# Kernel optimization log

Measured on AMD Instinct MI355X. Metric: run time of the kernel, lower is better.

Reference implementation:

```python
import jax, jax.numpy as jnp
import numpy as np

EPS = 1e-6
B, N, M, C, H = 4, 2048, 1024, 1024, 16
HD = C // H          # 64
HID = 4 * C          # 4096
SCALE = 1.0 / np.sqrt(HD)


def _ln(x, g, b):
    m = x.mean(-1, keepdims=True)
    v = jnp.mean((x - m) ** 2, -1, keepdims=True)
    return (x - m) * jax.lax.rsqrt(v + EPS) * g + b


def _rot(x):
    # interleaved rotate: (-x2, x1) pairs (rotate_half=False path)
    x1, x2 = x[..., ::2], x[..., 1::2]
    return jnp.stack([-x2, x1], axis=-1).reshape(x.shape)


def _apply_rope(x, emb):
    # emb: [N, 2*HD] = cat(sin, cos); x: [B,H,N,HD]
    sin, cos = jnp.split(emb, 2, axis=-1)
    return x * cos + _rot(x) * sin


def _sdpa(q, k, v):
    s = jnp.einsum('bhqd,bhkd->bhqk', q, k) * SCALE
    a = jax.nn.softmax(s, axis=-1)
    return jnp.einsum('bhqk,bhkd->bhqd', a, v)


def _forward(x, ctx, rope,
             wqkv, sa_qg, sa_qb, sa_kg, sa_kb, sa_wo, sa_bo,
             ca_wq, ca_wk, ca_wv, ca_qg, ca_qb, ca_kg, ca_kb, ca_wo, ca_bo, ca_gate,
             w1g, b1g, w1x, b1x, w2, b2, ls0, ls1, ls2):
    Bx, Nx, Cx = x.shape
    Mx = ctx.shape[1]
    # ---- self attention (fused QKV, qk-norm, RoPE) ----
    qkv = (x @ wqkv).reshape(Bx, Nx, 3, H, HD).transpose(2, 0, 3, 1, 4)  # [3,B,H,N,HD]
    q, k, v = qkv[0], qkv[1], qkv[2]
    q = _ln(q, sa_qg, sa_qb)
    k = _ln(k, sa_kg, sa_kb)
    q = _apply_rope(q, rope)
    k = _apply_rope(k, rope)
    sa = _sdpa(q, k, v).transpose(0, 2, 1, 3).reshape(Bx, Nx, Cx)
    sa = sa @ sa_wo + sa_bo
    x = ls0 * sa + x
    # ---- cross attention (GQA degenerate: n_kv_heads == n_q_heads), gated ----
    q = (x @ ca_wq).reshape(Bx, Nx, H, HD).transpose(0, 2, 1, 3)
    k = (ctx @ ca_wk).reshape(Bx, Mx, H, HD).transpose(0, 2, 1, 3)
    v = (ctx @ ca_wv).reshape(Bx, Mx, H, HD).transpose(0, 2, 1, 3)
    q = _ln(q, ca_qg, ca_qb)
    k = _ln(k, ca_kg, ca_kb)
    q = _apply_rope(q, rope)  # rope on queries only; ctx has its own positions
    ca = _sdpa(q, k, v).transpose(0, 2, 1, 3).reshape(Bx, Nx, Cx)
    ca = (ca @ ca_wo + ca_bo) * jnp.tanh(ca_gate)
    x = ls1 * ca + x
    # ---- SwiGLU FFN ----
    h = jax.nn.silu(x @ w1g + b1g) * (x @ w1x + b1x)
    f = h @ w2 + b2
    x = ls2 * f + x
    return x


def setup_inputs() -> dict:
    key = jax.random.key(0)
    ks = iter(jax.random.split(key, 32))
    rn = lambda shape, s=0.02: (jax.random.normal(next(ks), shape, jnp.float32) * s)
    inp = {
        'x': jax.random.normal(next(ks), (B, N, C), jnp.float32),
        'ctx': jax.random.normal(next(ks), (B, M, C), jnp.float32),
    }
    # rotary table: cat(sin, cos), interleaved-repeated freqs -> [N, 2*HD]
    pos = jnp.arange(N, dtype=jnp.float32)
    inv = 1.0 / (10000.0 ** (jnp.arange(0, HD, 2, dtype=jnp.float32) / HD))
    ang = pos[:, None] * inv[None, :]                      # [N, HD/2]
    sin = jnp.repeat(jnp.sin(ang), 2, axis=-1)
    cos = jnp.repeat(jnp.cos(ang), 2, axis=-1)
    inp['rope'] = jnp.concatenate([sin, cos], axis=-1)
    inp.update(
        wqkv=rn((C, 3 * C)),
        sa_qg=jnp.ones((HD,)), sa_qb=jnp.zeros((HD,)),
        sa_kg=jnp.ones((HD,)), sa_kb=jnp.zeros((HD,)),
        sa_wo=rn((C, C)), sa_bo=jnp.zeros((C,)),
        ca_wq=rn((C, C)), ca_wk=rn((C, C)), ca_wv=rn((C, C)),
        ca_qg=jnp.ones((HD,)), ca_qb=jnp.zeros((HD,)),
        ca_kg=jnp.ones((HD,)), ca_kb=jnp.zeros((HD,)),
        ca_wo=rn((C, C)), ca_bo=jnp.zeros((C,)),
        ca_gate=jnp.full((C,), 0.5, jnp.float32),
        w1g=rn((C, HID)), b1g=jnp.zeros((HID,)),
        w1x=rn((C, HID)), b1x=jnp.zeros((HID,)),
        w2=rn((HID, C)), b2=jnp.zeros((C,)),
        ls0=jnp.full((C,), 1e-5, jnp.float32),
        ls1=jnp.full((C,), 1e-5, jnp.float32),
        ls2=jnp.full((C,), 1e-5, jnp.float32),
    )
    return inp


def reference(x, ctx, rope,
              wqkv, sa_qg, sa_qb, sa_kg, sa_kb, sa_wo, sa_bo,
              ca_wq, ca_wk, ca_wv, ca_qg, ca_qb, ca_kg, ca_kb, ca_wo, ca_bo, ca_gate,
              w1g, b1g, w1x, b1x, w2, b2, ls0, ls1, ls2):
    return _forward(x, ctx, rope,
                    wqkv, sa_qg, sa_qb, sa_kg, sa_kb, sa_wo, sa_bo,
                    ca_wq, ca_wk, ca_wv, ca_qg, ca_qb, ca_kg, ca_kb, ca_wo, ca_bo, ca_gate,
                    w1g, b1g, w1x, b1x, w2, b2, ls0, ls1, ls2)
```

## Files before the change

### kernel.cpp

```cpp
#include <hip/hip_runtime.h>
#include <hip/hip_bf16.h>
#include <math.h>


typedef __attribute__((ext_vector_type(8))) short bf16x8;
typedef __attribute__((ext_vector_type(4))) short s16x4;
typedef __attribute__((ext_vector_type(4))) float f32x4;

#define DEV __device__ __forceinline__

DEV unsigned short f2us(float f) {
  __hip_bfloat16 h = __float2bfloat16(f);
  return __builtin_bit_cast(unsigned short, h);
}

DEV void gload_lds16(const void* g, void* l) {
  __builtin_amdgcn_global_load_lds((const __attribute__((address_space(1))) void*)g,
                                   (__attribute__((address_space(3))) void*)l, 16, 0, 0);
}

#define MFMA_BF16_16x16x32 __builtin_amdgcn_mfma_f32_16x16x32_bf16
#define WAITV0 asm volatile("s_waitcnt vmcnt(0)" ::: "memory")


__global__ __launch_bounds__(256) void cvt_f32_bf16(const float* __restrict__ in,
                                                    __hip_bfloat16* __restrict__ out,
                                                    long n) {
  long i = ((long)blockIdx.x * blockDim.x + threadIdx.x) * 4;
  if (i + 3 < n) {
    float4 v = *(const float4*)(in + i);
    out[i + 0] = __float2bfloat16(v.x);
    out[i + 1] = __float2bfloat16(v.y);
    out[i + 2] = __float2bfloat16(v.z);
    out[i + 3] = __float2bfloat16(v.w);
  }
}

__global__ __launch_bounds__(256) void transpose_cvt(const float* __restrict__ w,
                                                     __hip_bfloat16* __restrict__ wT,
                                                     int K, int N) {
  __shared__ float tile[32][33];
  int n0 = blockIdx.x * 32, k0 = blockIdx.y * 32;
  int tx = threadIdx.x, ty = threadIdx.y;
  #pragma unroll
  for (int i = 0; i < 32; i += 8)
    tile[ty + i][tx] = w[(long)(k0 + ty + i) * N + n0 + tx];
  __syncthreads();
  #pragma unroll
  for (int i = 0; i < 32; i += 8)
    wT[(long)(n0 + ty + i) * K + k0 + tx] = __float2bfloat16(tile[tx][ty + i]);
}

__global__ __launch_bounds__(256) void transpose_cvt_ilv(const float* __restrict__ w,
                                                         __hip_bfloat16* __restrict__ wI,
                                                         int K, int N, int ofs) {
  __shared__ float tile[32][33];
  int n0 = blockIdx.x * 32, k0 = blockIdx.y * 32;
  int tx = threadIdx.x, ty = threadIdx.y;
  #pragma unroll
  for (int i = 0; i < 32; i += 8)
    tile[ty + i][tx] = w[(long)(k0 + ty + i) * N + n0 + tx];
  __syncthreads();
  #pragma unroll
  for (int i = 0; i < 32; i += 8) {
    int j = n0 + ty + i;
    int r = 32 * (j >> 4) + (j & 15) + ofs;
    wI[(long)r * K + k0 + tx] = __float2bfloat16(tile[tx][ty + i]);
  }
}

__global__ __launch_bounds__(256) void transpose_v(const __hip_bfloat16* __restrict__ v,
                                                   long vBatch, long vRow,
                                                   __hip_bfloat16* __restrict__ vt,
                                                   int Nkv) {
  __shared__ unsigned short tile[32][36];
  int bh = blockIdx.z;
  int b = bh >> 4, h = bh & 15;
  int kv0 = blockIdx.x * 32;
  int d0 = blockIdx.y * 32;
  int tx = threadIdx.x, ty = threadIdx.y;
  const __hip_bfloat16* src = v + (long)b * vBatch + h * 64 + d0;
  #pragma unroll
  for (int i = 0; i < 32; i += 8)
    tile[ty + i][tx] = __builtin_bit_cast(unsigned short, src[(long)(kv0 + ty + i) * vRow + tx]);
  __syncthreads();
  unsigned short* dst = (unsigned short*)vt + ((long)bh * (Nkv >> 6) + (kv0 >> 6)) * 4608 + (kv0 & 32) + tx;
  #pragma unroll
  for (int i = 0; i < 32; i += 8)
    dst[(long)(d0 + ty + i) * 72] = tile[tx][ty + i];
}

__global__ __launch_bounds__(256) void ln_rope(__hip_bfloat16* __restrict__ buf,
                                               const float* __restrict__ rope,
                                               const float* __restrict__ g0,
                                               const float* __restrict__ b0,
                                               const float* __restrict__ g1,
                                               const float* __restrict__ b1,
                                               int Rows, int W,
                                               long rowStride, long whichStride,
                                               int ropeMask, long total) {
  int lane = threadIdx.x & 63;
  int wv = threadIdx.x >> 6;
  long id = (long)blockIdx.x * 4 + wv;
  if (id >= total) return;
  int which = (int)(id % W);
  long t = id / W;
  int h = (int)(t & 15); t >>= 4;
  int n = (int)(t % Rows);
  int b = (int)(t / Rows);
  __hip_bfloat16* p = buf + ((long)b * Rows + n) * rowStride + (long)which * whichStride + h * 64 + lane;
  float v = __bfloat162float(*p);
  float s = v;
  #pragma unroll
  for (int m = 32; m; m >>= 1) s += __shfl_xor(s, m);
  float mean = s * (1.f / 64.f);
  float d = v - mean;
  float q = d * d;
  #pragma unroll
  for (int m = 32; m; m >>= 1) q += __shfl_xor(q, m);
  float rstd = rsqrtf(q * (1.f / 64.f) + 1e-6f);
  const float* g = which ? g1 : g0;
  const float* bb = which ? b1 : b0;
  float xn = d * rstd * g[lane] + bb[lane];
  if ((ropeMask >> which) & 1) {
    float partner = __shfl_xor(xn, 1);
    float sn = rope[(long)n * 128 + lane];
    float cs = rope[(long)n * 128 + 64 + lane];
    xn = (lane & 1) ? (xn * cs + partner * sn) : (xn * cs - partner * sn);
  }
  *p = __float2bfloat16(xn);
}

template <int EPI>
DEV void epi_store(long idx, long col, float v,
                   float* __restrict__ out_f, __hip_bfloat16* __restrict__ out_b,
                   const float* __restrict__ bias, const float* __restrict__ scale,
                   const float* __restrict__ gate, const float* __restrict__ resid,
                   const __hip_bfloat16* __restrict__ mulin) {
  if constexpr (EPI == 0) {
    out_b[idx] = __float2bfloat16(v);
  } else if constexpr (EPI == 1) {
    float r = scale[col] * (v + bias[col]) + resid[idx];
    out_b[idx] = __float2bfloat16(r);
  } else if constexpr (EPI == 2) {
    float r = scale[col] * ((v + bias[col]) * tanhf(gate[col])) + __bfloat162float(mulin[idx]);
    out_b[idx] = __float2bfloat16(r);
  } else {
    out_f[idx] = scale[col] * (v + bias[col]) + __bfloat162float(mulin[idx]);
  }
}

template <int BM, int EPI>
__global__ __launch_bounds__(512, 2) void gemm2ph(const __hip_bfloat16* __restrict__ A,
                                                  const __hip_bfloat16* __restrict__ Bt,
                                                  int M, int N, int K,
                                                  float* __restrict__ out_f,
                                                  __hip_bfloat16* __restrict__ out_b,
                                                  const float* __restrict__ bias,
                                                  const float* __restrict__ scale,
                                                  const float* __restrict__ gate,
                                                  const float* __restrict__ resid,
                                                  const __hip_bfloat16* __restrict__ mulin) {
  constexpr int MF = BM / 32;
  constexpr int WRS = BM / 2;
  constexpr int AJ = BM * 8 / 512;
  __shared__ __align__(16) unsigned short As[2][BM * 64];
  __shared__ __align__(16) unsigned short Bs[2][256 * 64];

  int t = threadIdx.x;
  int l = t & 63, w = t >> 6;
  int lo = l & 15, hi = l >> 4;
  int wr = w >> 2, wc = w & 3;
  long bm = blockIdx.x, bn = blockIdx.y;
  const __hip_bfloat16* Ab = A + bm * BM * (long)K;
  const __hip_bfloat16* Bb = Bt + bn * 256 * (long)K;
  int nt = K >> 6;

  auto stage = [&](int kt, int buf) {
    long kb = (long)kt * 64;
    #pragma unroll
    for (int j = 0; j < AJ; j++) {
      int q = j * 512 + t;
      int row = q >> 3, c = (q & 7) ^ (row & 7);
      gload_lds16(Ab + (long)row * K + kb + c * 8, &As[buf][q * 8]);
    }
    #pragma unroll
    for (int j = 0; j < 4; j++) {
      int q = j * 512 + t;
      int row = q >> 3, c = (q & 7) ^ (row & 7);
      gload_lds16(Bb + (long)row * K + kb + c * 8, &Bs[buf][q * 8]);
    }
  };

  f32x4 acc[MF][4] = {};

  stage(0, 0);
  WAITV0;
  __builtin_amdgcn_s_barrier();

  for (int kt = 0; kt < nt; ++kt) {
    int cur = kt & 1;
    if (kt + 1 < nt) stage(kt + 1, cur ^ 1);

    #pragma unroll
    for (int ks = 0; ks < 2; ks++) {
      bf16x8 bfrag[4];
      #pragma unroll
      for (int n = 0; n < 4; n++) {
        int rb = wc * 64 + n * 16 + lo;
        bfrag[n] = *(const bf16x8*)&Bs[cur][rb * 64 + (((ks << 2) | hi) ^ (rb & 7)) * 8];
      }
      #pragma unroll
      for (int mg = 0; mg < MF; mg += 4) {
        bf16x8 afrag[4];
        #pragma unroll
        for (int m = 0; m < 4; m++) {
          int ra = wr * WRS + (mg + m) * 16 + lo;
          afrag[m] = *(const bf16x8*)&As[cur][ra * 64 + (((ks << 2) | hi) ^ (ra & 7)) * 8];
        }
        __builtin_amdgcn_s_setprio(1);
        #pragma unroll
        for (int m = 0; m < 4; m++)
          #pragma unroll
          for (int n = 0; n < 4; n++)
            acc[mg + m][n] = MFMA_BF16_16x16x32(afrag[m], bfrag[n], acc[mg + m][n], 0, 0, 0);
        __builtin_amdgcn_s_setprio(0);
      }
    }

    if (kt + 1 < nt) {
      WAITV0;
      __builtin_amdgcn_s_barrier();
    }
  }

  if constexpr (EPI == 6) {
    #pragma unroll
    for (int m = 0; m < MF; m++)
      #pragma unroll
      for (int np = 0; np < 2; np++)
        #pragma unroll
        for (int i = 0; i < 4; i++) {
          long row = bm * BM + wr * WRS + m * 16 + hi * 4 + i;
          long jc = bn * 128 + wc * 32 + np * 16 + lo;
          float g = acc[m][np * 2][i] + bias[jc];
          float xv = acc[m][np * 2 + 1][i] + gate[jc];
          float hv = (g / (1.f + expf(-g))) * xv;
          out_b[row * (long)(N >> 1) + jc] = __float2bfloat16(hv);
        }
  } else {
    #pragma unroll
    for (int m = 0; m < MF; m++)
      #pragma unroll
      for (int n = 0; n < 4; n++)
        #pragma unroll
        for (int i = 0; i < 4; i++) {
          long row = bm * BM + wr * WRS + m * 16 + hi * 4 + i;
          long col = bn * 256 + wc * 64 + n * 16 + lo;
          epi_store<EPI>(row * (long)N + col, col, acc[m][n][i],
                         out_f, out_b, bias, scale, gate, resid, mulin);
        }
  }
}

__global__ __launch_bounds__(256) void attn32(const __hip_bfloat16* __restrict__ qB, long qBatch, long qRow,
                                              const __hip_bfloat16* __restrict__ kB, long kBatch, long kRow,
                                              const __hip_bfloat16* __restrict__ vt,
                                              __hip_bfloat16* __restrict__ out, int Nq, int Nkv) {
  const float SC2 = 0.125f * 1.44269504089f;
  int t = threadIdx.x;
  int l = t & 63, w = t >> 6;
  int lo = l & 15, hi = l >> 4;
  int nQC = Nq >> 7;
  int qc = blockIdx.x % nQC;
  int bh = blockIdx.x / nQC;
  int h = bh & 15, b = bh >> 4;
  int q0 = qc * 128 + w * 32;

  __shared__ unsigned short P_all[4][32 * 72];
  __shared__ unsigned short V_lds[2][64 * 72];
  unsigned short* P = P_all[w];

  bf16x8 qf[2][2];
#pragma unroll
  for (int qs = 0; qs < 2; qs++) {
    const __hip_bfloat16* qp = qB + (long)b * qBatch + (long)(q0 + qs * 16 + lo) * qRow + h * 64 + hi * 8;
    qf[qs][0] = *(const bf16x8*)qp;
    qf[qs][1] = *(const bf16x8*)(qp + 32);
  }

  float mrow[2] = {-INFINITY, -INFINITY};
  float lsum[2] = {0.f, 0.f};
  f32x4 acc[2][4] = {};
  const f32x4 fz = {0.f, 0.f, 0.f, 0.f};

  const __hip_bfloat16* kbase = kB + (long)b * kBatch + h * 64 + hi * 8;
  int nt = Nkv >> 6;
  const char* vtb = (const char*)vt + (long)bh * nt * 9216;

  auto stageV = [&](int tile, unsigned short* dstb) {
    const char* src = vtb + (long)tile * 9216;
    gload_lds16(src + t * 16, &dstb[t * 8]);
    gload_lds16(src + (t + 256) * 16, &dstb[(t + 256) * 8]);
    if (t < 64) gload_lds16(src + (t + 512) * 16, &dstb[(t + 512) * 8]);
  };
  auto loadK = [&](int tile, bf16x8 (&kg)[4][2]) {
#pragma unroll
    for (int g = 0; g < 4; g++) {
      const __hip_bfloat16* kp = kbase + (long)(tile * 64 + g * 16 + lo) * kRow;
      kg[g][0] = *(const bf16x8*)kp;
      kg[g][1] = *(const bf16x8*)(kp + 32);
    }
  };
  auto qkt = [&](bf16x8 (&kg)[4][2], f32x4 (&ST)[2][4]) {
    __builtin_amdgcn_s_setprio(1);
#pragma unroll
    for (int qs = 0; qs < 2; qs++)
#pragma unroll
      for (int g = 0; g < 4; g++) {
        f32x4 s0 = MFMA_BF16_16x16x32(kg[g][0], qf[qs][0], fz, 0, 0, 0);
        ST[qs][g] = MFMA_BF16_16x16x32(kg[g][1], qf[qs][1], s0, 0, 0, 0);
      }
    __builtin_amdgcn_s_setprio(0);
  };
  auto smax = [&](f32x4 (&ST)[2][4]) {
#pragma unroll
    for (int qs = 0; qs < 2; qs++) {
      float mg0 = fmaxf(fmaxf(ST[qs][0][0], ST[qs][0][1]), fmaxf(ST[qs][0][2], ST[qs][0][3]));
      float mg1 = fmaxf(fmaxf(ST[qs][1][0], ST[qs][1][1]), fmaxf(ST[qs][1][2], ST[qs][1][3]));
      float mg2 = fmaxf(fmaxf(ST[qs][2][0], ST[qs][2][1]), fmaxf(ST[qs][2][2], ST[qs][2][3]));
      float mg3 = fmaxf(fmaxf(ST[qs][3][0], ST[qs][3][1]), fmaxf(ST[qs][3][2], ST[qs][3][3]));
      float rm = fmaxf(fmaxf(mg0, mg1), fmaxf(mg2, mg3)) * SC2;
      rm = fmaxf(rm, __shfl_xor(rm, 16));
      rm = fmaxf(rm, __shfl_xor(rm, 32));
      if (!__all(rm <= mrow[qs] + 8.f)) {
        float mn = fmaxf(mrow[qs], rm);
        float scl = exp2f(mrow[qs] - mn);
        mrow[qs] = mn;
        lsum[qs] *= scl;
        float c0 = __shfl(scl, hi * 4 + 0);
        float c1 = __shfl(scl, hi * 4 + 1);
        float c2 = __shfl(scl, hi * 4 + 2);
        float c3 = __shfl(scl, hi * 4 + 3);
#pragma unroll
        for (int tt = 0; tt < 4; tt++) {
          acc[qs][tt][0] *= c0; acc[qs][tt][1] *= c1;
          acc[qs][tt][2] *= c2; acc[qs][tt][3] *= c3;
        }
      }
      float m = mrow[qs];
      float rs = 0.f;
#pragma unroll
      for (int g = 0; g < 4; g++) {
        float p0 = exp2f(fmaf(ST[qs][g][0], SC2, -m));
        float p1 = exp2f(fmaf(ST[qs][g][1], SC2, -m));
        float p2 = exp2f(fmaf(ST[qs][g][2], SC2, -m));
        float p3 = exp2f(fmaf(ST[qs][g][3], SC2, -m));
        rs += (p0 + p1) + (p2 + p3);
        s16x4 pw;
        pw[0] = (short)f2us(p0); pw[1] = (short)f2us(p1);
        pw[2] = (short)f2us(p2); pw[3] = (short)f2us(p3);
        *(s16x4*)&P[(qs * 16 + lo) * 72 + g * 16 + hi * 4] = pw;
      }
      rs += __shfl_xor(rs, 16);
      rs += __shfl_xor(rs, 32);
      lsum[qs] += rs;
    }
  };
  auto pv = [&](const unsigned short* Vb) {
    bf16x8 pf[2][2];
#pragma unroll
    for (int qs = 0; qs < 2; qs++) {
      pf[qs][0] = *(const bf16x8*)&P[(qs * 16 + lo) * 72 + hi * 8];
      pf[qs][1] = *(const bf16x8*)&P[(qs * 16 + lo) * 72 + 32 + hi * 8];
    }
    __builtin_amdgcn_s_setprio(1);
#pragma unroll
    for (int tt = 0; tt < 4; tt++) {
      bf16x8 v0 = *(const bf16x8*)&Vb[(tt * 16 + lo) * 72 + hi * 8];
      bf16x8 v1 = *(const bf16x8*)&Vb[(tt * 16 + lo) * 72 + 32 + hi * 8];
#pragma unroll
      for (int qs = 0; qs < 2; qs++) {
        acc[qs][tt] = MFMA_BF16_16x16x32(pf[qs][0], v0, acc[qs][tt], 0, 0, 0);
        acc[qs][tt] = MFMA_BF16_16x16x32(pf[qs][1], v1, acc[qs][tt], 0, 0, 0);
      }
    }
    __builtin_amdgcn_s_setprio(0);
  };

  bf16x8 kgA[4][2], kgB[4][2];
  stageV(0, V_lds[0]);
  loadK(0, kgA);

  for (int it = 0; it < nt; it += 2) {
    __syncthreads();
    stageV(it + 1, V_lds[1]);
    f32x4 ST0[2][4];
    qkt(kgA, ST0);
    loadK(it + 1, kgB);
    smax(ST0);
    pv(V_lds[0]);

    __syncthreads();
    if (it + 2 < nt) stageV(it + 2, V_lds[0]);
    f32x4 ST1[2][4];
    qkt(kgB, ST1);
    if (it + 2 < nt) loadK(it + 2, kgA);
    smax(ST1);
    pv(V_lds[1]);
  }

#pragma unroll
  for (int qs = 0; qs < 2; qs++) {
    float inv = 1.f / lsum[qs];
    float iv0 = __shfl(inv, hi * 4 + 0);
    float iv1 = __shfl(inv, hi * 4 + 1);
    float iv2 = __shfl(inv, hi * 4 + 2);
    float iv3 = __shfl(inv, hi * 4 + 3);
    float iv[4] = {iv0, iv1, iv2, iv3};
#pragma unroll
    for (int i = 0; i < 4; i++) {
      long row = q0 + qs * 16 + hi * 4 + i;
      __hip_bfloat16* op = out + ((long)b * Nq + row) * 1024 + h * 64 + lo;
#pragma unroll
      for (int tt = 0; tt < 4; tt++) op[tt * 16] = __float2bfloat16(acc[qs][tt][i] * iv[i]);
    }
  }
}


extern "C" void kernel_launch(void* const* d_in, const int* in_sizes, int n_in,
                              void* d_out, int out_size, void* d_ws, size_t ws_size,
                              hipStream_t stream) {
  (void)in_sizes; (void)n_in; (void)out_size; (void)ws_size;

  const float* x      = (const float*)d_in[0];
  const float* ctx    = (const float*)d_in[1];
  const float* rope   = (const float*)d_in[2];
  const float* wqkv   = (const float*)d_in[3];
  const float* sa_qg  = (const float*)d_in[4];
  const float* sa_qb  = (const float*)d_in[5];
  const float* sa_kg  = (const float*)d_in[6];
  const float* sa_kb  = (const float*)d_in[7];
  const float* sa_wo  = (const float*)d_in[8];
  const float* sa_bo  = (const float*)d_in[9];
  const float* ca_wq  = (const float*)d_in[10];
  const float* ca_wk  = (const float*)d_in[11];
  const float* ca_wv  = (const float*)d_in[12];
  const float* ca_qg  = (const float*)d_in[13];
  const float* ca_qb  = (const float*)d_in[14];
  const float* ca_kg  = (const float*)d_in[15];
  const float* ca_kb  = (const float*)d_in[16];
  const float* ca_wo  = (const float*)d_in[17];
  const float* ca_bo  = (const float*)d_in[18];
  const float* ca_gate= (const float*)d_in[19];
  const float* w1g    = (const float*)d_in[20];
  const float* b1g    = (const float*)d_in[21];
  const float* w1x    = (const float*)d_in[22];
  const float* b1x    = (const float*)d_in[23];
  const float* w2     = (const float*)d_in[24];
  const float* b2     = (const float*)d_in[25];
  const float* ls0    = (const float*)d_in[26];
  const float* ls1    = (const float*)d_in[27];
  const float* ls2    = (const float*)d_in[28];

  char* ws = (char*)d_ws;

  const long OFF_WQKVT = 0;
  const long OFF_SAWOT = 6291456;
  const long OFF_CAWQT = 8388608;
  const long OFF_CAWKT = 10485760;
  const long OFF_CAWVT = 12582912;
  const long OFF_CAWOT = 14680064;
  const long OFF_W1I   = 16777216;
  const long OFF_W2T   = 33554432;
  const long OFF_XB    = 41943040;
  const long OFF_QC    = OFF_XB;
  const long OFF_CTXB  = 58720256;
  const long OFF_QKV   = 67108864;
  const long OFF_CAO   = 67108864;
  const long OFF_X2B   = 83886080;
  const long OFF_SG    = 100663296;
  const long OFF_SAO   = 117440512;
  const long OFF_KVC   = 117440512;
  const long OFF_CAVT  = 134217728;
  const long OFF_X1B   = 167772160;
  const long OFF_SAVT  = 184549376;

  auto bfp = [&](long off) { return (__hip_bfloat16*)(ws + off); };

  dim3 tb32(32, 8);
  transpose_cvt<<<dim3(96, 32), tb32, 0, stream>>>(wqkv,  bfp(OFF_WQKVT), 1024, 3072);
  transpose_cvt<<<dim3(32, 32), tb32, 0, stream>>>(sa_wo, bfp(OFF_SAWOT), 1024, 1024);
  transpose_cvt<<<dim3(32, 32), tb32, 0, stream>>>(ca_wq, bfp(OFF_CAWQT), 1024, 1024);
  transpose_cvt<<<dim3(32, 32), tb32, 0, stream>>>(ca_wk, bfp(OFF_CAWKT), 1024, 1024);
  transpose_cvt<<<dim3(32, 32), tb32, 0, stream>>>(ca_wv, bfp(OFF_CAWVT), 1024, 1024);
  transpose_cvt<<<dim3(32, 32), tb32, 0, stream>>>(ca_wo, bfp(OFF_CAWOT), 1024, 1024);
  transpose_cvt_ilv<<<dim3(128, 32), tb32, 0, stream>>>(w1g, bfp(OFF_W1I), 1024, 4096, 0);
  transpose_cvt_ilv<<<dim3(128, 32), tb32, 0, stream>>>(w1x, bfp(OFF_W1I), 1024, 4096, 16);
  transpose_cvt<<<dim3(32, 128), tb32, 0, stream>>>(w2,   bfp(OFF_W2T), 4096, 1024);

  cvt_f32_bf16<<<8192, 256, 0, stream>>>(x,   bfp(OFF_XB),   8388608);
  cvt_f32_bf16<<<4096, 256, 0, stream>>>(ctx, bfp(OFF_CTXB), 4194304);

  gemm2ph<128, 0><<<dim3(64, 12), 512, 0, stream>>>(bfp(OFF_XB), bfp(OFF_WQKVT), 8192, 3072, 1024,
                                                    nullptr, bfp(OFF_QKV), nullptr, nullptr, nullptr, nullptr, nullptr);

  transpose_v<<<dim3(64, 2, 64), tb32, 0, stream>>>(bfp(OFF_QKV) + 2048, (long)2048 * 3072, 3072,
                                                    bfp(OFF_SAVT), 2048);

  ln_rope<<<65536, 256, 0, stream>>>(bfp(OFF_QKV), rope, sa_qg, sa_qb, sa_kg, sa_kb,
                                     2048, 2, 3 * 1024, 1024, 3, (long)4 * 2048 * 16 * 2);

  attn32<<<1024, 256, 0, stream>>>(bfp(OFF_QKV),        (long)2048 * 3072, 3072,
                                   bfp(OFF_QKV) + 1024, (long)2048 * 3072, 3072,
                                   bfp(OFF_SAVT), bfp(OFF_SAO), 2048, 2048);

  gemm2ph<128, 1><<<dim3(64, 4), 512, 0, stream>>>(bfp(OFF_SAO), bfp(OFF_SAWOT), 8192, 1024, 1024,
                                                   nullptr, bfp(OFF_X1B), sa_bo, ls0, nullptr, x, nullptr);

  gemm2ph<128, 0><<<dim3(64, 4), 512, 0, stream>>>(bfp(OFF_X1B), bfp(OFF_CAWQT), 8192, 1024, 1024,
                                                   nullptr, bfp(OFF_QC), nullptr, nullptr, nullptr, nullptr, nullptr);
  gemm2ph<128, 0><<<dim3(32, 8), 512, 0, stream>>>(bfp(OFF_CTXB), bfp(OFF_CAWKT), 4096, 2048, 1024,
                                                   nullptr, bfp(OFF_KVC), nullptr, nullptr, nullptr, nullptr, nullptr);

  transpose_v<<<dim3(32, 2, 64), tb32, 0, stream>>>(bfp(OFF_KVC) + 1024, (long)1024 * 2048, 2048,
                                                    bfp(OFF_CAVT), 1024);

  ln_rope<<<32768, 256, 0, stream>>>(bfp(OFF_QC), rope, ca_qg, ca_qb, ca_qg, ca_qb,
                                     2048, 1, 1024, 0, 1, (long)4 * 2048 * 16);
  ln_rope<<<16384, 256, 0, stream>>>(bfp(OFF_KVC), rope, ca_kg, ca_kb, ca_kg, ca_kb,
                                     1024, 1, 2048, 0, 0, (long)4 * 1024 * 16);

  attn32<<<1024, 256, 0, stream>>>(bfp(OFF_QC), (long)2048 * 1024, 1024,
                                   bfp(OFF_KVC), (long)1024 * 2048, 2048,
                                   bfp(OFF_CAVT), bfp(OFF_CAO), 2048, 1024);

  gemm2ph<128, 2><<<dim3(64, 4), 512, 0, stream>>>(bfp(OFF_CAO), bfp(OFF_CAWOT), 8192, 1024, 1024,
                                                   nullptr, bfp(OFF_X2B), ca_bo, ls1, ca_gate, nullptr,
                                                   bfp(OFF_X1B));

  gemm2ph<256, 6><<<dim3(32, 32), 512, 0, stream>>>(bfp(OFF_X2B), bfp(OFF_W1I), 8192, 8192, 1024,
                                                    nullptr, bfp(OFF_SG), b1g, nullptr, b1x, nullptr, nullptr);

  gemm2ph<128, 5><<<dim3(64, 4), 512, 0, stream>>>(bfp(OFF_SG), bfp(OFF_W2T), 8192, 1024, 4096,
                                                   (float*)d_out, nullptr, b2, ls2, nullptr, nullptr,
                                                   bfp(OFF_X2B));
}
```

Baseline: 842.8 us.

## Fuse per-head LayerNorm and RoPE into projection GEMM epilogues

Adds GEMM epilogue variants that compute per-head LayerNorm (with a 16-lane shuffle reduction across each wave's 64-column head slice) and interleaved RoPE directly on the accumulators. These replace the three separate ln_rope kernel launches for the self-attention QKV, cross-attention Q and cross-attention K/V projections. The goal is to remove the extra read-modify-write passes over the Q/K buffers and the launch overhead. In exchange the epilogues carry more register pressure and shuffles, and the rope table is passed through the out_f pointer.

```diff
diff --git a/kernel.cpp b/kernel.cpp
--- a/kernel.cpp
+++ b/kernel.cpp
@@ -90,47 +90,6 @@
     dst[(long)(d0 + ty + i) * 72] = tile[tx][ty + i];
 }
 
-__global__ __launch_bounds__(256) void ln_rope(__hip_bfloat16* __restrict__ buf,
-                                               const float* __restrict__ rope,
-                                               const float* __restrict__ g0,
-                                               const float* __restrict__ b0,
-                                               const float* __restrict__ g1,
-                                               const float* __restrict__ b1,
-                                               int Rows, int W,
-                                               long rowStride, long whichStride,
-                                               int ropeMask, long total) {
-  int lane = threadIdx.x & 63;
-  int wv = threadIdx.x >> 6;
-  long id = (long)blockIdx.x * 4 + wv;
-  if (id >= total) return;
-  int which = (int)(id % W);
-  long t = id / W;
-  int h = (int)(t & 15); t >>= 4;
-  int n = (int)(t % Rows);
-  int b = (int)(t / Rows);
-  __hip_bfloat16* p = buf + ((long)b * Rows + n) * rowStride + (long)which * whichStride + h * 64 + lane;
-  float v = __bfloat162float(*p);
-  float s = v;
-  #pragma unroll
-  for (int m = 32; m; m >>= 1) s += __shfl_xor(s, m);
-  float mean = s * (1.f / 64.f);
-  float d = v - mean;
-  float q = d * d;
-  #pragma unroll
-  for (int m = 32; m; m >>= 1) q += __shfl_xor(q, m);
-  float rstd = rsqrtf(q * (1.f / 64.f) + 1e-6f);
-  const float* g = which ? g1 : g0;
-  const float* bb = which ? b1 : b0;
-  float xn = d * rstd * g[lane] + bb[lane];
-  if ((ropeMask >> which) & 1) {
-    float partner = __shfl_xor(xn, 1);
-    float sn = rope[(long)n * 128 + lane];
-    float cs = rope[(long)n * 128 + 64 + lane];
-    xn = (lane & 1) ? (xn * cs + partner * sn) : (xn * cs - partner * sn);
-  }
-  *p = __float2bfloat16(xn);
-}
-
 template <int EPI>
 DEV void epi_store(long idx, long col, float v,
                    float* __restrict__ out_f, __hip_bfloat16* __restrict__ out_b,
@@ -248,6 +207,69 @@
           float hv = (g / (1.f + expf(-g))) * xv;
           out_b[row * (long)(N >> 1) + jc] = __float2bfloat16(hv);
         }
+  } else if constexpr (EPI == 8 || EPI == 9 || EPI == 10) {
+    int colbase = (int)(bn * 256 + wc * 64);
+    int slice = colbase >> 10;
+    bool doln;
+    const float *gv_p, *bv_p;
+    if constexpr (EPI == 8) {
+      doln = (slice < 2);
+      gv_p = (slice == 0) ? bias : gate;
+      bv_p = (slice == 0) ? scale : resid;
+    } else if constexpr (EPI == 9) {
+      doln = true; gv_p = bias; bv_p = scale;
+    } else {
+      doln = (slice == 0); gv_p = bias; bv_p = scale;
+    }
+    if (!doln) {
+      #pragma unroll
+      for (int m = 0; m < MF; m++)
+        #pragma unroll
+        for (int n = 0; n < 4; n++)
+          #pragma unroll
+          for (int i = 0; i < 4; i++) {
+            long row = bm * BM + wr * WRS + m * 16 + hi * 4 + i;
+            out_b[row * (long)N + colbase + n * 16 + lo] = __float2bfloat16(acc[m][n][i]);
+          }
+    } else {
+      float gv[4], bv[4];
+      #pragma unroll
+      for (int nn = 0; nn < 4; nn++) {
+        gv[nn] = gv_p[nn * 16 + lo];
+        bv[nn] = bv_p[nn * 16 + lo];
+      }
+      #pragma unroll
+      for (int m = 0; m < MF; m++)
+        #pragma unroll
+        for (int i = 0; i < 4; i++) {
+          float v0 = acc[m][0][i], v1 = acc[m][1][i], v2 = acc[m][2][i], v3 = acc[m][3][i];
+          float s = (v0 + v1) + (v2 + v3);
+          s += __shfl_xor(s, 1); s += __shfl_xor(s, 2);
+          s += __shfl_xor(s, 4); s += __shfl_xor(s, 8);
+          float mean = s * 0.015625f;
+          float d0 = v0 - mean, d1 = v1 - mean, d2 = v2 - mean, d3 = v3 - mean;
+          float q2 = (d0 * d0 + d1 * d1) + (d2 * d2 + d3 * d3);
+          q2 += __shfl_xor(q2, 1); q2 += __shfl_xor(q2, 2);
+          q2 += __shfl_xor(q2, 4); q2 += __shfl_xor(q2, 8);
+          float rstd = rsqrtf(q2 * 0.015625f + 1e-6f);
+          long row = bm * BM + wr * WRS + m * 16 + hi * 4 + i;
+          int nseq = (int)(row & 2047);
+          float xs0 = d0 * rstd, xs1 = d1 * rstd, xs2 = d2 * rstd, xs3 = d3 * rstd;
+          float xsv[4] = {xs0, xs1, xs2, xs3};
+          #pragma unroll
+          for (int nn = 0; nn < 4; nn++) {
+            float xn = xsv[nn] * gv[nn] + bv[nn];
+            if constexpr (EPI != 10) {
+              float partner = __shfl_xor(xn, 1);
+              int d = nn * 16 + lo;
+              float sn = out_f[(long)nseq * 128 + d];
+              float cs = out_f[(long)nseq * 128 + 64 + d];
+              xn = (lo & 1) ? (xn * cs + partner * sn) : (xn * cs - partner * sn);
+            }
+            out_b[row * (long)N + colbase + nn * 16 + lo] = __float2bfloat16(xn);
+          }
+        }
+    }
   } else {
     #pragma unroll
     for (int m = 0; m < MF; m++)
@@ -503,14 +525,12 @@
   cvt_f32_bf16<<<8192, 256, 0, stream>>>(x,   bfp(OFF_XB),   8388608);
   cvt_f32_bf16<<<4096, 256, 0, stream>>>(ctx, bfp(OFF_CTXB), 4194304);
 
-  gemm2ph<128, 0><<<dim3(64, 12), 512, 0, stream>>>(bfp(OFF_XB), bfp(OFF_WQKVT), 8192, 3072, 1024,
-                                                    nullptr, bfp(OFF_QKV), nullptr, nullptr, nullptr, nullptr, nullptr);
+  gemm2ph<128, 8><<<dim3(64, 12), 512, 0, stream>>>(bfp(OFF_XB), bfp(OFF_WQKVT), 8192, 3072, 1024,
+                                                    (float*)rope, bfp(OFF_QKV),
+                                                    sa_qg, sa_qb, sa_kg, sa_kb, nullptr);
 
   transpose_v<<<dim3(64, 2, 64), tb32, 0, stream>>>(bfp(OFF_QKV) + 2048, (long)2048 * 3072, 3072,
                                                     bfp(OFF_SAVT), 2048);
-
-  ln_rope<<<65536, 256, 0, stream>>>(bfp(OFF_QKV), rope, sa_qg, sa_qb, sa_kg, sa_kb,
-                                     2048, 2, 3 * 1024, 1024, 3, (long)4 * 2048 * 16 * 2);
 
   attn32<<<1024, 256, 0, stream>>>(bfp(OFF_QKV),        (long)2048 * 3072, 3072,
                                    bfp(OFF_QKV) + 1024, (long)2048 * 3072, 3072,
@@ -519,18 +539,15 @@
   gemm2ph<128, 1><<<dim3(64, 4), 512, 0, stream>>>(bfp(OFF_SAO), bfp(OFF_SAWOT), 8192, 1024, 1024,
                                                    nullptr, bfp(OFF_X1B), sa_bo, ls0, nullptr, x, nullptr);
 
-  gemm2ph<128, 0><<<dim3(64, 4), 512, 0, stream>>>(bfp(OFF_X1B), bfp(OFF_CAWQT), 8192, 1024, 1024,
-                                                   nullptr, bfp(OFF_QC), nullptr, nullptr, nullptr, nullptr, nullptr);
-  gemm2ph<128, 0><<<dim3(32, 8), 512, 0, stream>>>(bfp(OFF_CTXB), bfp(OFF_CAWKT), 4096, 2048, 1024,
-                                                   nullptr, bfp(OFF_KVC), nullptr, nullptr, nullptr, nullptr, nullptr);
+  gemm2ph<128, 9><<<dim3(64, 4), 512, 0, stream>>>(bfp(OFF_X1B), bfp(OFF_CAWQT), 8192, 1024, 1024,
+                                                   (float*)rope, bfp(OFF_QC),
+                                                   ca_qg, ca_qb, nullptr, nullptr, nullptr);
+  gemm2ph<128, 10><<<dim3(32, 8), 512, 0, stream>>>(bfp(OFF_CTXB), bfp(OFF_CAWKT), 4096, 2048, 1024,
+                                                    nullptr, bfp(OFF_KVC),
+                                                    ca_kg, ca_kb, nullptr, nullptr, nullptr);
 
   transpose_v<<<dim3(32, 2, 64), tb32, 0, stream>>>(bfp(OFF_KVC) + 1024, (long)1024 * 2048, 2048,
                                                     bfp(OFF_CAVT), 1024);
-
-  ln_rope<<<32768, 256, 0, stream>>>(bfp(OFF_QC), rope, ca_qg, ca_qb, ca_qg, ca_qb,
-                                     2048, 1, 1024, 0, 1, (long)4 * 2048 * 16);
-  ln_rope<<<16384, 256, 0, stream>>>(bfp(OFF_KVC), rope, ca_kg, ca_kb, ca_kg, ca_kb,
-                                     1024, 1, 2048, 0, 0, (long)4 * 1024 * 16);
 
   attn32<<<1024, 256, 0, stream>>>(bfp(OFF_QC), (long)2048 * 1024, 1024,
                                    bfp(OFF_KVC), (long)1024 * 2048, 2048,
```

Result: faster. 749.2 us (-11.1%).
